# Performance work log

Hardware: AMD Instinct MI355X
Metric: run time of the kernel (lower is better)

## Reference

```python
import jax, jax.numpy as jnp
import numpy as np

EMBED_DIM = 512
NUM_HEADS = 8
HEAD_DIM = EMBED_DIM // NUM_HEADS


def setup_inputs() -> dict:
    key = jax.random.key(0)
    ks = jax.random.split(key, 6)
    B, S, E = 2, 4096, EMBED_DIM
    scale = 1.0 / np.sqrt(E)
    return {
        "rotation_params": jax.random.normal(ks[0], (E, E), jnp.float32) * scale,
        "entangle_params": jax.random.normal(ks[1], (E, E), jnp.float32) * scale,
        "inputs": jax.random.normal(ks[2], (B, S, E), jnp.float32),
        "w_q": jax.random.normal(ks[3], (E, E), jnp.float32) * scale,
        "w_k": jax.random.normal(ks[4], (E, E), jnp.float32) * scale,
        "w_v": jax.random.normal(ks[5], (E, E), jnp.float32) * scale,
    }


def reference(rotation_params, entangle_params, inputs, w_q, w_k, w_v):
    B, S, E = inputs.shape
    H, D = NUM_HEADS, HEAD_DIM
    # torch nn.Linear(x) = x @ W.T ; then extra matmul with rotation/entangle mats
    q = (inputs @ w_q.T) @ rotation_params  # [B,S,E]
    k = (inputs @ w_k.T) @ entangle_params  # [B,S,E]
    v = inputs @ w_v.T                       # [B,S,E]
    # split heads -> [B,H,S,D]
    q = q.reshape(B, S, H, D).transpose(0, 2, 1, 3)
    k = k.reshape(B, S, H, D).transpose(0, 2, 1, 3)
    v = v.reshape(B, S, H, D).transpose(0, 2, 1, 3)
    scores = jnp.einsum("bhqd,bhkd->bhqk", q, k) / jnp.sqrt(jnp.float32(D))
    attn = jax.nn.softmax(scores, axis=-1)  # dropout p=0 (eval) -> identity
    out = jnp.einsum("bhqk,bhkd->bhqd", attn, v)
    return out.transpose(0, 2, 1, 3).reshape(B, S, E)
```

## Files before the change

kernel.cpp:

```cpp
#include <hip/hip_runtime.h>
#include <cstddef>

#define E 512
#define H 8
#define D 64
#define BATCH 2
#define SEQ 4096

typedef __attribute__((ext_vector_type(8))) short bf16x8;
typedef __attribute__((ext_vector_type(4))) float f32x4;

__device__ __forceinline__ ushort f2bf(float f) {
  unsigned u = __builtin_bit_cast(unsigned, f);
  u += 0x7fff + ((u >> 16) & 1);
  return (ushort)(u >> 16);
}
__device__ __forceinline__ float bf2f(ushort h) {
  return __builtin_bit_cast(float, (unsigned)h << 16);
}
__device__ __forceinline__ unsigned pk_bf16(float lo, float hi) {
#if __has_builtin(__builtin_amdgcn_cvt_pk_bf16_f32)
  typedef __attribute__((ext_vector_type(2))) __bf16 bfv2;
  bfv2 r = __builtin_amdgcn_cvt_pk_bf16_f32(lo, hi);
  return __builtin_bit_cast(unsigned, r);
#else
  return (unsigned)f2bf(lo) | ((unsigned)f2bf(hi) << 16);
#endif
}
__device__ __forceinline__ float fexp2(float x) {
#if __has_builtin(__builtin_amdgcn_exp2f)
  return __builtin_amdgcn_exp2f(x);
#else
  return exp2f(x);
#endif
}

__global__ __launch_bounds__(256) void xcast(const float* __restrict__ x,
                                             ushort* __restrict__ xh,
                                             ushort* __restrict__ xl) {
  size_t i = ((size_t)blockIdx.x * 256 + threadIdx.x) * 4;
  float4 v = *(const float4*)&x[i];
  ushort4 h, l;
  h.x = f2bf(v.x); l.x = f2bf(v.x - bf2f(h.x));
  h.y = f2bf(v.y); l.y = f2bf(v.y - bf2f(h.y));
  h.z = f2bf(v.z); l.z = f2bf(v.z - bf2f(h.z));
  h.w = f2bf(v.w); l.w = f2bf(v.w - bf2f(h.w));
  *(ushort4*)&xh[i] = h;
  *(ushort4*)&xl[i] = l;
}

__global__ __launch_bounds__(256) void fold_tiled(
    const float* __restrict__ wq, const float* __restrict__ wk,
    const float* __restrict__ rot, const float* __restrict__ ent,
    ushort* __restrict__ weffbT) {
  const int which = blockIdx.z;
  const float* w = which ? wk : wq;
  const float* r = which ? ent : rot;
  const int k = blockIdx.x * 256 + threadIdx.x;
  const int n0 = blockIdx.y * 8;
  float acc[8] = {};
  for (int j0 = 0; j0 < E; j0 += 16) {
    float wv_[16];
#pragma unroll
    for (int u = 0; u < 16; ++u) wv_[u] = w[(size_t)(j0 + u) * E + k];
#pragma unroll
    for (int u = 0; u < 16; ++u)
#pragma unroll
      for (int t = 0; t < 8; ++t)
        acc[t] += wv_[u] * r[(size_t)(j0 + u) * E + n0 + t];
  }
#pragma unroll
  for (int t = 0; t < 8; ++t)
    weffbT[(size_t)which * E * E + (size_t)(n0 + t) * E + k] = f2bf(acc[t]);
}

__global__ __launch_bounds__(256) void wv_cast(const float* __restrict__ wv,
                                               ushort* __restrict__ dst) {
  size_t i = ((size_t)blockIdx.x * 256 + threadIdx.x) * 4;
  float4 v = *(const float4*)&wv[i];
  ushort4 o;
  o.x = f2bf(v.x); o.y = f2bf(v.y); o.z = f2bf(v.z); o.w = f2bf(v.w);
  *(ushort4*)&dst[i] = o;
}

#define LDA 40

__global__ __launch_bounds__(256) void qkv_fused(
    const ushort* __restrict__ xhg, const ushort* __restrict__ xlg,
    const ushort* __restrict__ weffbT, ushort* __restrict__ qg,
    ushort* __restrict__ kg, ushort* __restrict__ vtg) {
  __shared__ ushort sm[5 * 64 * LDA];
  ushort* Ah = sm;
  ushort* Al = sm + 64 * LDA;
  ushort* Bs = sm + 2 * 64 * LDA;
  ushort* vt_tile = Bs;

  const int head = blockIdx.x;
  const int m0 = blockIdx.y * 64;
  const int tid = threadIdx.x;
  const int wave = tid >> 6, lane = tid & 63;
  const int l15 = lane & 15, quad = lane >> 4;
  const int ar = tid >> 2, ac8 = (tid & 3) * 8;

  const ushort* arow = xhg + (size_t)(m0 + ar) * E + ac8;
  const ushort* lrow = xlg + (size_t)(m0 + ar) * E + ac8;
  const ushort* b0row = weffbT + (size_t)(head * 64 + ar) * E + ac8;

  f32x4 acc[3][4];
#pragma unroll
  for (int w = 0; w < 3; ++w)
#pragma unroll
    for (int nt = 0; nt < 4; ++nt) acc[w][nt] = (f32x4){0.f, 0.f, 0.f, 0.f};

  uint4 pa_h = *(const uint4*)&arow[0];
  uint4 pa_l = *(const uint4*)&lrow[0];
  uint4 pb0 = *(const uint4*)&b0row[0];
  uint4 pb1 = *(const uint4*)&b0row[E * E];
  uint4 pb2 = *(const uint4*)&b0row[2 * E * E];

  for (int k0 = 0; k0 < E; k0 += 32) {
    __syncthreads();
    *(uint4*)&Ah[ar * LDA + ac8] = pa_h;
    *(uint4*)&Al[ar * LDA + ac8] = pa_l;
    *(uint4*)&Bs[0 * 64 * LDA + ar * LDA + ac8] = pb0;
    *(uint4*)&Bs[1 * 64 * LDA + ar * LDA + ac8] = pb1;
    *(uint4*)&Bs[2 * 64 * LDA + ar * LDA + ac8] = pb2;
    __syncthreads();

    const int kn = (k0 + 32 < E) ? k0 + 32 : 0;
    pa_h = *(const uint4*)&arow[kn];
    pa_l = *(const uint4*)&lrow[kn];
    pb0 = *(const uint4*)&b0row[kn];
    pb1 = *(const uint4*)&b0row[E * E + kn];
    pb2 = *(const uint4*)&b0row[2 * E * E + kn];

    bf16x8 ah = *(const bf16x8*)&Ah[(wave * 16 + l15) * LDA + quad * 8];
    bf16x8 al = *(const bf16x8*)&Al[(wave * 16 + l15) * LDA + quad * 8];
#pragma unroll
    for (int w = 0; w < 3; ++w)
#pragma unroll
      for (int nt = 0; nt < 4; ++nt) {
        bf16x8 bf = *(const bf16x8*)&Bs[w * 64 * LDA + (nt * 16 + l15) * LDA +
                                        quad * 8];
        acc[w][nt] =
            __builtin_amdgcn_mfma_f32_16x16x32_bf16(ah, bf, acc[w][nt], 0, 0, 0);
        acc[w][nt] =
            __builtin_amdgcn_mfma_f32_16x16x32_bf16(al, bf, acc[w][nt], 0, 0, 0);
      }
  }

  const int b = m0 >> 12;
  const int s_base = m0 & (SEQ - 1);
  const float QSCALE = 0.125f * 1.44269504f;

#pragma unroll
  for (int w = 0; w < 2; ++w) {
    ushort* dst = (w == 0) ? qg : kg;
    float sc = (w == 0) ? QSCALE : 1.0f;
#pragma unroll
    for (int nt = 0; nt < 4; ++nt)
#pragma unroll
      for (int r = 0; r < 4; ++r) {
        float v = acc[w][nt][r] * sc;
        float vo = __shfl_xor(v, 1);
        if (!(lane & 1)) {
          int s = s_base + wave * 16 + quad * 4 + r;
          size_t ix = ((size_t)(b * H + head) * SEQ + s) * D + nt * 16 + l15;
          *(unsigned*)&dst[ix] = pk_bf16(v, vo);
        }
      }
  }

  __syncthreads();
#pragma unroll
  for (int nt = 0; nt < 4; ++nt) {
    uint2 w2;
    w2.x = pk_bf16(acc[2][nt][0], acc[2][nt][1]);
    w2.y = pk_bf16(acc[2][nt][2], acc[2][nt][3]);
    *(uint2*)&vt_tile[(nt * 16 + l15) * 72 + wave * 16 + quad * 4] = w2;
  }
  __syncthreads();
  {
    int vr = tid >> 2, vs = (tid & 3) * 16;
    uint4 c0 = *(const uint4*)&vt_tile[vr * 72 + vs];
    uint4 c1 = *(const uint4*)&vt_tile[vr * 72 + vs + 8];
    size_t vo = ((size_t)(b * H + head) * D + vr) * SEQ + s_base + vs;
    *(uint4*)&vtg[vo] = c0;
    *(uint4*)&vtg[vo + 8] = c1;
  }
}

#define LDK 72

__global__ __launch_bounds__(512, 4) void attn_mfma(
    const ushort* __restrict__ qg, const ushort* __restrict__ kg,
    const ushort* __restrict__ vtg, float* __restrict__ out) {
  __shared__ ushort Ks[2][64 * LDK];
  __shared__ ushort Vs[2][64 * LDK];
  __shared__ ushort Ps[8 * 32 * LDK];
  __shared__ float lex[128];

  const int qt = blockIdx.x;
  const int bh = blockIdx.y;
  const int tid = threadIdx.x;
  const int wave = tid >> 6;
  const int grp = wave >> 2, wq = wave & 3;
  const int lane = tid & 63;
  const int l15 = lane & 15, quad = lane >> 4;
  const int gtid = tid & 255;

  const ushort* qp = qg + (size_t)bh * SEQ * D;
  const ushort* kp = kg + (size_t)bh * SEQ * D;
  const ushort* vp = vtg + (size_t)bh * D * SEQ;
  ushort* Psw = Ps + wave * 32 * LDK;
  ushort* Ksg = Ks[grp];
  ushort* Vsg = Vs[grp];

  const int qrow0 = qt * 128 + wq * 32;
  bf16x8 qf[2][2];
#pragma unroll
  for (int sub = 0; sub < 2; ++sub)
#pragma unroll
    for (int ks = 0; ks < 2; ++ks)
      qf[sub][ks] = *(const bf16x8*)&qp[(size_t)(qrow0 + sub * 16 + l15) * D +
                                        ks * 32 + quad * 8];

  f32x4 o[2][4];
#pragma unroll
  for (int sub = 0; sub < 2; ++sub)
#pragma unroll
    for (int nt = 0; nt < 4; ++nt) o[sub][nt] = (f32x4){0.f, 0.f, 0.f, 0.f};
  float l_r[2] = {0.f, 0.f};

  const int r0 = gtid >> 3, c0 = (gtid & 7) * 8;
  const int r1 = 32 + r0;

  uint4 pk0 = *(const uint4*)&kp[(size_t)grp * 64 * D + r0 * 64 + c0];
  uint4 pk1 = *(const uint4*)&kp[(size_t)grp * 64 * D + r1 * 64 + c0];
  uint4 pv0 = *(const uint4*)&vp[(size_t)r0 * SEQ + grp * 64 + c0];
  uint4 pv1 = *(const uint4*)&vp[(size_t)r1 * SEQ + grp * 64 + c0];

  for (int it = 0; it < SEQ / 128; ++it) {
    __syncthreads();
    *(uint4*)&Ksg[r0 * LDK + c0] = pk0;
    *(uint4*)&Ksg[r1 * LDK + c0] = pk1;
    *(uint4*)&Vsg[r0 * LDK + c0] = pv0;
    *(uint4*)&Vsg[r1 * LDK + c0] = pv1;
    __syncthreads();

    {
      const int itn = (it + 1 < SEQ / 128) ? it + 1 : it;
      const int ktn = itn * 2 + grp;
      const ushort* ksrc = kp + (size_t)ktn * 64 * D;
      pk0 = *(const uint4*)&ksrc[r0 * 64 + c0];
      pk1 = *(const uint4*)&ksrc[r1 * 64 + c0];
      pv0 = *(const uint4*)&vp[(size_t)r0 * SEQ + ktn * 64 + c0];
      pv1 = *(const uint4*)&vp[(size_t)r1 * SEQ + ktn * 64 + c0];
    }

    f32x4 st[2][4];
#pragma unroll
    for (int sub = 0; sub < 2; ++sub)
#pragma unroll
      for (int knt = 0; knt < 4; ++knt)
        st[sub][knt] = (f32x4){0.f, 0.f, 0.f, 0.f};
#pragma unroll
    for (int knt = 0; knt < 4; ++knt)
#pragma unroll
      for (int ks = 0; ks < 2; ++ks) {
        bf16x8 kf =
            *(const bf16x8*)&Ksg[(knt * 16 + l15) * LDK + ks * 32 + quad * 8];
        st[0][knt] = __builtin_amdgcn_mfma_f32_16x16x32_bf16(
            kf, qf[0][ks], st[0][knt], 0, 0, 0);
        st[1][knt] = __builtin_amdgcn_mfma_f32_16x16x32_bf16(
            kf, qf[1][ks], st[1][knt], 0, 0, 0);
      }

#pragma unroll
    for (int sub = 0; sub < 2; ++sub) {
      float rs = 0.f;
#pragma unroll
      for (int knt = 0; knt < 4; ++knt) {
        float p0 = fexp2(st[sub][knt][0]);
        float p1 = fexp2(st[sub][knt][1]);
        float p2 = fexp2(st[sub][knt][2]);
        float p3 = fexp2(st[sub][knt][3]);
        rs += (p0 + p1) + (p2 + p3);
        uint2 w2;
        w2.x = pk_bf16(p0, p1);
        w2.y = pk_bf16(p2, p3);
        *(uint2*)&Psw[(sub * 16 + l15) * LDK + knt * 16 + quad * 4] = w2;
      }
      l_r[sub] += rs;
    }
    __asm__ volatile("s_waitcnt lgkmcnt(0)" ::: "memory");

    bf16x8 pf[2][2];
#pragma unroll
    for (int sub = 0; sub < 2; ++sub)
#pragma unroll
      for (int ks = 0; ks < 2; ++ks)
        pf[sub][ks] = *(const bf16x8*)&Psw[(sub * 16 + l15) * LDK + ks * 32 +
                                           quad * 8];
#pragma unroll
    for (int nt = 0; nt < 4; ++nt)
#pragma unroll
      for (int ks = 0; ks < 2; ++ks) {
        bf16x8 vf =
            *(const bf16x8*)&Vsg[(nt * 16 + l15) * LDK + ks * 32 + quad * 8];
        o[0][nt] = __builtin_amdgcn_mfma_f32_16x16x32_bf16(pf[0][ks], vf,
                                                           o[0][nt], 0, 0, 0);
        o[1][nt] = __builtin_amdgcn_mfma_f32_16x16x32_bf16(pf[1][ks], vf,
                                                           o[1][nt], 0, 0, 0);
      }
  }

  __syncthreads();
  float lsum[2];
#pragma unroll
  for (int sub = 0; sub < 2; ++sub) {
    float l = l_r[sub];
    l += __shfl_xor(l, 16);
    l += __shfl_xor(l, 32);
    lsum[sub] = l;
  }
  float* Oex = (float*)Ps;
  if (grp == 1) {
#pragma unroll
    for (int sub = 0; sub < 2; ++sub)
#pragma unroll
      for (int nt = 0; nt < 4; ++nt)
#pragma unroll
        for (int r = 0; r < 4; ++r)
          Oex[(wq * 32 + sub * 16 + quad * 4 + r) * 68 + nt * 16 + l15] =
              o[sub][nt][r];
    if (quad == 0) {
      lex[wq * 32 + l15] = lsum[0];
      lex[wq * 32 + 16 + l15] = lsum[1];
    }
  }
  __syncthreads();
  if (grp == 0) {
    const int b = bh >> 3, h = bh & 7;
#pragma unroll
    for (int sub = 0; sub < 2; ++sub) {
      float l = lsum[sub] + lex[wq * 32 + sub * 16 + l15];
      float linv = 1.f / l;
      float inv_r[4];
#pragma unroll
      for (int r = 0; r < 4; ++r) inv_r[r] = __shfl(linv, quad * 4 + r);
#pragma unroll
      for (int nt = 0; nt < 4; ++nt)
#pragma unroll
        for (int r = 0; r < 4; ++r) {
          int row = wq * 32 + sub * 16 + quad * 4 + r;
          float val = o[sub][nt][r] + Oex[row * 68 + nt * 16 + l15];
          int srow = qt * 128 + row;
          out[((size_t)b * SEQ + srow) * E + h * D + nt * 16 + l15] =
              val * inv_r[r];
        }
    }
  }
}

extern "C" void kernel_launch(void* const* d_in, const int* in_sizes, int n_in,
                              void* d_out, int out_size, void* d_ws,
                              size_t ws_size, hipStream_t stream) {
  const float* rot = (const float*)d_in[0];
  const float* ent = (const float*)d_in[1];
  const float* x = (const float*)d_in[2];
  const float* wq = (const float*)d_in[3];
  const float* wk = (const float*)d_in[4];
  const float* wv = (const float*)d_in[5];
  float* out = (float*)d_out;

  const size_t NX = (size_t)BATCH * SEQ * E;
  ushort* weffbT = (ushort*)d_ws;
  ushort* xh = weffbT + 3 * E * E;
  ushort* xl = xh + NX;
  ushort* qg = xl + NX;
  ushort* kg = qg + NX;
  ushort* vtg = kg + NX;

  xcast<<<dim3(NX / 1024), 256, 0, stream>>>(x, xh, xl);
  fold_tiled<<<dim3(E / 256, E / 8, 2), 256, 0, stream>>>(wq, wk, rot, ent,
                                                          weffbT);
  wv_cast<<<dim3(E * E / 1024), 256, 0, stream>>>(wv, weffbT + 2 * E * E);
  qkv_fused<<<dim3(H, BATCH * SEQ / 64), 256, 0, stream>>>(xh, xl, weffbT, qg,
                                                           kg, vtg);
  attn_mfma<<<dim3(SEQ / 128, BATCH * H), 512, 0, stream>>>(qg, kg, vtg, out);
}
```

Measured before the change: 256.0 us.

## Switch attention to 32x32x16 MFMA and keep P in registers via permlane swap

Rewrites the attention inner loop to use 32x32x16 bf16 MFMAs computing S transposed, then converts the exponentiated scores directly into A-operand fragments with v_permlane32_swap instead of storing P to shared memory and reading it back. This removes the per-wave P LDS buffer and its round trip, shrinks shared memory, and adds s_setprio around MFMA sections. Occupancy hint is lowered from 4 to 3 blocks per CU, which likely reflects higher register pressure from the 16-wide accumulators. The row-sum and epilogue are reworked for the 32x32 output layout.

```diff
diff --git a/kernel.cpp b/kernel.cpp
--- a/kernel.cpp
+++ b/kernel.cpp
@@ -9,6 +9,8 @@
 
 typedef __attribute__((ext_vector_type(8))) short bf16x8;
 typedef __attribute__((ext_vector_type(4))) float f32x4;
+typedef __attribute__((ext_vector_type(16))) float f32x16;
+typedef __attribute__((ext_vector_type(4))) unsigned uint4v;
 
 __device__ __forceinline__ ushort f2bf(float f) {
   unsigned u = __builtin_bit_cast(unsigned, f);
@@ -33,6 +35,9 @@
 #else
   return exp2f(x);
 #endif
+}
+__device__ __forceinline__ void permswap32(unsigned& a, unsigned& b) {
+  asm volatile("v_permlane32_swap_b32 %0, %1" : "+v"(a), "+v"(b));
 }
 
 __global__ __launch_bounds__(256) void xcast(const float* __restrict__ x,
@@ -192,13 +197,13 @@
 
 #define LDK 72
 
-__global__ __launch_bounds__(512, 4) void attn_mfma(
+__global__ __launch_bounds__(512, 3) void attn_mfma(
     const ushort* __restrict__ qg, const ushort* __restrict__ kg,
     const ushort* __restrict__ vtg, float* __restrict__ out) {
-  __shared__ ushort Ks[2][64 * LDK];
-  __shared__ ushort Vs[2][64 * LDK];
-  __shared__ ushort Ps[8 * 32 * LDK];
-  __shared__ float lex[128];
+  __shared__ ushort sm[4 * 64 * LDK + 256];
+  ushort* Ks0 = sm;
+  ushort* Vs0 = sm + 2 * 64 * LDK;
+  float* lex = (float*)(sm + 4 * 64 * LDK);
 
   const int qt = blockIdx.x;
   const int bh = blockIdx.y;
@@ -206,31 +211,26 @@
   const int wave = tid >> 6;
   const int grp = wave >> 2, wq = wave & 3;
   const int lane = tid & 63;
-  const int l15 = lane & 15, quad = lane >> 4;
+  const int l31 = lane & 31, hi = lane >> 5;
   const int gtid = tid & 255;
 
   const ushort* qp = qg + (size_t)bh * SEQ * D;
   const ushort* kp = kg + (size_t)bh * SEQ * D;
   const ushort* vp = vtg + (size_t)bh * D * SEQ;
-  ushort* Psw = Ps + wave * 32 * LDK;
-  ushort* Ksg = Ks[grp];
-  ushort* Vsg = Vs[grp];
+  ushort* Ksg = Ks0 + grp * 64 * LDK;
+  ushort* Vsg = Vs0 + grp * 64 * LDK;
 
   const int qrow0 = qt * 128 + wq * 32;
-  bf16x8 qf[2][2];
-#pragma unroll
-  for (int sub = 0; sub < 2; ++sub)
-#pragma unroll
-    for (int ks = 0; ks < 2; ++ks)
-      qf[sub][ks] = *(const bf16x8*)&qp[(size_t)(qrow0 + sub * 16 + l15) * D +
-                                        ks * 32 + quad * 8];
-
-  f32x4 o[2][4];
-#pragma unroll
-  for (int sub = 0; sub < 2; ++sub)
-#pragma unroll
-    for (int nt = 0; nt < 4; ++nt) o[sub][nt] = (f32x4){0.f, 0.f, 0.f, 0.f};
-  float l_r[2] = {0.f, 0.f};
+  bf16x8 qf[4];
+#pragma unroll
+  for (int ds = 0; ds < 4; ++ds)
+    qf[ds] =
+        *(const bf16x8*)&qp[(size_t)(qrow0 + l31) * D + ds * 16 + hi * 8];
+
+  f32x16 o[2];
+  o[0] = 0.f;
+  o[1] = 0.f;
+  float l_r = 0.f;
 
   const int r0 = gtid >> 3, c0 = (gtid & 7) * 8;
   const int r1 = 32 + r0;
@@ -258,107 +258,95 @@
       pv1 = *(const uint4*)&vp[(size_t)r1 * SEQ + ktn * 64 + c0];
     }
 
-    f32x4 st[2][4];
-#pragma unroll
-    for (int sub = 0; sub < 2; ++sub)
-#pragma unroll
-      for (int knt = 0; knt < 4; ++knt)
-        st[sub][knt] = (f32x4){0.f, 0.f, 0.f, 0.f};
-#pragma unroll
-    for (int knt = 0; knt < 4; ++knt)
-#pragma unroll
-      for (int ks = 0; ks < 2; ++ks) {
+#pragma unroll
+    for (int t = 0; t < 2; ++t) {
+      f32x16 st = 0.f;
+      __builtin_amdgcn_s_setprio(1);
+#pragma unroll
+      for (int ds = 0; ds < 4; ++ds) {
         bf16x8 kf =
-            *(const bf16x8*)&Ksg[(knt * 16 + l15) * LDK + ks * 32 + quad * 8];
-        st[0][knt] = __builtin_amdgcn_mfma_f32_16x16x32_bf16(
-            kf, qf[0][ks], st[0][knt], 0, 0, 0);
-        st[1][knt] = __builtin_amdgcn_mfma_f32_16x16x32_bf16(
-            kf, qf[1][ks], st[1][knt], 0, 0, 0);
-      }
-
-#pragma unroll
-    for (int sub = 0; sub < 2; ++sub) {
-      float rs = 0.f;
-#pragma unroll
-      for (int knt = 0; knt < 4; ++knt) {
-        float p0 = fexp2(st[sub][knt][0]);
-        float p1 = fexp2(st[sub][knt][1]);
-        float p2 = fexp2(st[sub][knt][2]);
-        float p3 = fexp2(st[sub][knt][3]);
-        rs += (p0 + p1) + (p2 + p3);
-        uint2 w2;
-        w2.x = pk_bf16(p0, p1);
-        w2.y = pk_bf16(p2, p3);
-        *(uint2*)&Psw[(sub * 16 + l15) * LDK + knt * 16 + quad * 4] = w2;
-      }
-      l_r[sub] += rs;
+            *(const bf16x8*)&Ksg[(t * 32 + l31) * LDK + ds * 16 + hi * 8];
+        st = __builtin_amdgcn_mfma_f32_32x32x16_bf16(kf, qf[ds], st, 0, 0, 0);
+      }
+      __builtin_amdgcn_s_setprio(0);
+
+      float pv[16];
+#pragma unroll
+      for (int r = 0; r < 16; ++r) pv[r] = fexp2(st[r]);
+      {
+        float s01 = (pv[0] + pv[1]) + (pv[2] + pv[3]);
+        float s23 = (pv[4] + pv[5]) + (pv[6] + pv[7]);
+        float s45 = (pv[8] + pv[9]) + (pv[10] + pv[11]);
+        float s67 = (pv[12] + pv[13]) + (pv[14] + pv[15]);
+        l_r += (s01 + s23) + (s45 + s67);
+      }
+
+      unsigned w0[4], w1[4];
+#pragma unroll
+      for (int j = 0; j < 2; ++j) {
+        {
+          unsigned c0w = pk_bf16(pv[2 * j + 0], pv[2 * j + 1]);
+          unsigned c1w = pk_bf16(pv[2 * j + 4], pv[2 * j + 5]);
+          permswap32(c0w, c1w);
+          w0[j] = c0w;
+          w0[2 + j] = c1w;
+        }
+        {
+          unsigned c0w = pk_bf16(pv[2 * j + 8], pv[2 * j + 9]);
+          unsigned c1w = pk_bf16(pv[2 * j + 12], pv[2 * j + 13]);
+          permswap32(c0w, c1w);
+          w1[j] = c0w;
+          w1[2 + j] = c1w;
+        }
+      }
+      bf16x8 pf0 =
+          __builtin_bit_cast(bf16x8, (uint4v){w0[0], w0[1], w0[2], w0[3]});
+      bf16x8 pf1 =
+          __builtin_bit_cast(bf16x8, (uint4v){w1[0], w1[1], w1[2], w1[3]});
+
+      __builtin_amdgcn_s_setprio(1);
+#pragma unroll
+      for (int nt = 0; nt < 2; ++nt) {
+        bf16x8 vf0 =
+            *(const bf16x8*)&Vsg[(nt * 32 + l31) * LDK + t * 32 + hi * 8];
+        o[nt] = __builtin_amdgcn_mfma_f32_32x32x16_bf16(pf0, vf0, o[nt], 0, 0,
+                                                        0);
+        bf16x8 vf1 = *(const bf16x8*)&Vsg[(nt * 32 + l31) * LDK + t * 32 + 16 +
+                                          hi * 8];
+        o[nt] = __builtin_amdgcn_mfma_f32_32x32x16_bf16(pf1, vf1, o[nt], 0, 0,
+                                                        0);
+      }
+      __builtin_amdgcn_s_setprio(0);
     }
-    __asm__ volatile("s_waitcnt lgkmcnt(0)" ::: "memory");
-
-    bf16x8 pf[2][2];
-#pragma unroll
-    for (int sub = 0; sub < 2; ++sub)
-#pragma unroll
-      for (int ks = 0; ks < 2; ++ks)
-        pf[sub][ks] = *(const bf16x8*)&Psw[(sub * 16 + l15) * LDK + ks * 32 +
-                                           quad * 8];
-#pragma unroll
-    for (int nt = 0; nt < 4; ++nt)
-#pragma unroll
-      for (int ks = 0; ks < 2; ++ks) {
-        bf16x8 vf =
-            *(const bf16x8*)&Vsg[(nt * 16 + l15) * LDK + ks * 32 + quad * 8];
-        o[0][nt] = __builtin_amdgcn_mfma_f32_16x16x32_bf16(pf[0][ks], vf,
-                                                           o[0][nt], 0, 0, 0);
-        o[1][nt] = __builtin_amdgcn_mfma_f32_16x16x32_bf16(pf[1][ks], vf,
-                                                           o[1][nt], 0, 0, 0);
-      }
   }
 
   __syncthreads();
-  float lsum[2];
-#pragma unroll
-  for (int sub = 0; sub < 2; ++sub) {
-    float l = l_r[sub];
-    l += __shfl_xor(l, 16);
-    l += __shfl_xor(l, 32);
-    lsum[sub] = l;
-  }
-  float* Oex = (float*)Ps;
+  float lg = l_r + __shfl_xor(l_r, 32);
+  float* Oex = (float*)sm;
   if (grp == 1) {
 #pragma unroll
-    for (int sub = 0; sub < 2; ++sub)
-#pragma unroll
-      for (int nt = 0; nt < 4; ++nt)
-#pragma unroll
-        for (int r = 0; r < 4; ++r)
-          Oex[(wq * 32 + sub * 16 + quad * 4 + r) * 68 + nt * 16 + l15] =
-              o[sub][nt][r];
-    if (quad == 0) {
-      lex[wq * 32 + l15] = lsum[0];
-      lex[wq * 32 + 16 + l15] = lsum[1];
-    }
+    for (int nt = 0; nt < 2; ++nt)
+#pragma unroll
+      for (int r = 0; r < 16; ++r) {
+        int row = (r & 3) + 8 * (r >> 2) + 4 * hi;
+        Oex[(wq * 32 + row) * 68 + nt * 32 + l31] = o[nt][r];
+      }
+    if (lane < 32) lex[wq * 32 + l31] = lg;
   }
   __syncthreads();
   if (grp == 0) {
+    float linv = 1.f / (lg + lex[wq * 32 + l31]);
     const int b = bh >> 3, h = bh & 7;
 #pragma unroll
-    for (int sub = 0; sub < 2; ++sub) {
-      float l = lsum[sub] + lex[wq * 32 + sub * 16 + l15];
-      float linv = 1.f / l;
-      float inv_r[4];
-#pragma unroll
-      for (int r = 0; r < 4; ++r) inv_r[r] = __shfl(linv, quad * 4 + r);
-#pragma unroll
-      for (int nt = 0; nt < 4; ++nt)
-#pragma unroll
-        for (int r = 0; r < 4; ++r) {
-          int row = wq * 32 + sub * 16 + quad * 4 + r;
-          float val = o[sub][nt][r] + Oex[row * 68 + nt * 16 + l15];
-          int srow = qt * 128 + row;
-          out[((size_t)b * SEQ + srow) * E + h * D + nt * 16 + l15] =
-              val * inv_r[r];
-        }
+    for (int r = 0; r < 16; ++r) {
+      int row = (r & 3) + 8 * (r >> 2) + 4 * hi;
+      float inv = __shfl(linv, row);
+      int srow = qt * 128 + wq * 32 + row;
+#pragma unroll
+      for (int nt = 0; nt < 2; ++nt) {
+        float val = o[nt][r] + Oex[(wq * 32 + row) * 68 + nt * 32 + l31];
+        out[((size_t)b * SEQ + srow) * E + h * D + nt * 32 + l31] = val * inv;
+      }
     }
   }
 }
```

Measured after the change: 246.6 us. 3.6% less time.
